# Kernel tuning notes

Hardware: AMD Instinct MI355X
Metric: run time of the kernel (lower is better)

Reference implementation:

```python
import jax, jax.numpy as jnp
import numpy as np
import math

D_MODEL = 1024
N_HEADS = 16
D_HEAD = D_MODEL // N_HEADS
LSR_RANK = 32
B, T = 4, 2048


def setup_inputs() -> dict:
    key = jax.random.key(0)
    ks = jax.random.split(key, 11)
    s = 1.0 / math.sqrt(D_MODEL)
    x = jax.random.normal(ks[0], (B, T, D_MODEL), dtype=jnp.float32)
    Wq = jax.random.uniform(ks[1], (D_MODEL, D_MODEL), minval=-s, maxval=s)
    bq = jax.random.uniform(ks[2], (D_MODEL,), minval=-s, maxval=s)
    Wk = jax.random.uniform(ks[3], (D_MODEL, D_MODEL), minval=-s, maxval=s)
    bk = jax.random.uniform(ks[4], (D_MODEL,), minval=-s, maxval=s)
    Wv = jax.random.uniform(ks[5], (D_MODEL, D_MODEL), minval=-s, maxval=s)
    bv = jax.random.uniform(ks[6], (D_MODEL,), minval=-s, maxval=s)
    Wo = jax.random.uniform(ks[7], (D_MODEL, D_MODEL), minval=-s, maxval=s)
    bo = jax.random.uniform(ks[8], (D_MODEL,), minval=-s, maxval=s)
    Wq_lsr = jax.random.normal(ks[9], (N_HEADS, D_HEAD, LSR_RANK)) / math.sqrt(D_HEAD)
    Wk_lsr = jax.random.normal(ks[10], (N_HEADS, D_HEAD, LSR_RANK)) / math.sqrt(D_HEAD)
    return {"x": x, "Wq": Wq, "bq": bq, "Wk": Wk, "bk": bk,
            "Wv": Wv, "bv": bv, "Wo": Wo, "bo": bo,
            "Wq_lsr": Wq_lsr, "Wk_lsr": Wk_lsr}


def reference(x, Wq, bq, Wk, bk, Wv, bv, Wo, bo, Wq_lsr, Wk_lsr):
    Bq, Tq, _ = x.shape
    # Linear projections (torch Linear: x @ W.T + b), split into heads -> (B,H,T,Dh)
    def split_heads(y):
        return y.reshape(Bq, Tq, N_HEADS, D_HEAD).transpose(0, 2, 1, 3)
    q = split_heads(x @ Wq.T + bq)
    k = split_heads(x @ Wk.T + bk)
    v = split_heads(x @ Wv.T + bv)
    # LSR: project q,k to rank-R per head
    q_lr = jnp.einsum('bhtd,hdr->bhtr', q, Wq_lsr)
    k_lr = jnp.einsum('bhtd,hdr->bhtr', k, Wk_lsr)
    scale = 1.0 / math.sqrt(max(LSR_RANK, 1))
    scores = jnp.einsum('bhir,bhjr->bhij', q_lr, k_lr) * scale  # (B,H,T,T)
    causal_mask = jnp.triu(jnp.ones((Tq, Tq), dtype=bool), k=1)
    scores = jnp.where(causal_mask, jnp.float32(-jnp.inf), scores)
    attn = jax.nn.softmax(scores, axis=-1)
    y = jnp.einsum('bhij,bhjd->bhid', attn, v)  # (B,H,T,Dh)
    y = y.transpose(0, 2, 1, 3).reshape(Bq, Tq, D_MODEL)
    return y @ Wo.T + bo
```

## Files before the change

kernel.cpp:

```cpp
#include <hip/hip_runtime.h>

#define B_  4
#define T_  2048
#define H_  16
#define DM_ 1024
#define DH_ 64
#define RK_ 32

using u16 = unsigned short;
using u32 = unsigned int;
typedef float  floatx4 __attribute__((ext_vector_type(4)));
typedef __bf16 bf16x8  __attribute__((ext_vector_type(8)));
typedef u16    u16x8   __attribute__((ext_vector_type(8)));
typedef u16    u16x4   __attribute__((ext_vector_type(4)));
typedef short  s16x4   __attribute__((ext_vector_type(4)));

#define MFMA16(a,b,c) __builtin_amdgcn_mfma_f32_16x16x32_bf16((a),(b),(c),0,0,0)
#define MFMA1K(a,b,c) __builtin_amdgcn_mfma_f32_16x16x16bf16_1k((a),(b),(c),0,0,0)

__device__ __forceinline__ u16 f2bf(float f) {
  unsigned u = __float_as_uint(f);
  u += 0x7fffu + ((u >> 16) & 1u);
  return (u16)(u >> 16);
}
__device__ __forceinline__ u32 pack_bf(float a, float b) {
  u32 ua = __float_as_uint(a); ua += 0x7fffu + ((ua >> 16) & 1u);
  u32 ub = __float_as_uint(b); ub += 0x7fffu + ((ub >> 16) & 1u);
  return __builtin_amdgcn_perm(ub, ua, 0x07060302u);
}
__device__ __forceinline__ u32 tpack(float a, float b) {
  return __builtin_amdgcn_perm(__float_as_uint(b), __float_as_uint(a), 0x07060302u);
}

__device__ __forceinline__ void async_copy16(const u16* g, const u16* lds_uniform_base) {
  __builtin_amdgcn_global_load_lds(
      (const __attribute__((address_space(1))) unsigned int*)(unsigned long long)g,
      (__attribute__((address_space(3))) unsigned int*)(unsigned int)(unsigned long long)lds_uniform_base,
      16, 0, 0);
}

__global__ __launch_bounds__(256) void cvt_x(const float* __restrict__ s,
                                             u16* __restrict__ d, int n4) {
  int i = blockIdx.x * 256 + threadIdx.x;
  if (i >= n4) return;
  float4 v = reinterpret_cast<const float4*>(s)[i];
  u16x4 o = { f2bf(v.x), f2bf(v.y), f2bf(v.z), f2bf(v.w) };
  reinterpret_cast<u16x4*>(d)[i] = o;
}

__global__ __launch_bounds__(256) void cvt_wvo(const float* __restrict__ Wv,
                                               const float* __restrict__ Wo,
                                               u16* __restrict__ Wcat) {
  int i = blockIdx.x * 256 + threadIdx.x;
  int reg = i >> 18;
  const float* s = reg ? Wo : Wv;
  int j = i & 262143;
  float4 v = reinterpret_cast<const float4*>(s)[j];
  u16x4 o = { f2bf(v.x), f2bf(v.y), f2bf(v.z), f2bf(v.w) };
  reinterpret_cast<u16x4*>(Wcat)[(reg ? 524288 : 0) + j] = o;
}

__global__ __launch_bounds__(256) void lsr_fold(const float* __restrict__ W,
                                                const float* __restrict__ bias,
                                                const float* __restrict__ lsr,
                                                float fold,
                                                u16* __restrict__ Weff,
                                                float* __restrict__ beff) {
  const int hr = blockIdx.x;
  const int h = hr >> 5, r = hr & 31;
  const int tid = threadIdx.x;
  __shared__ float lw[64];
  if (tid < 64) lw[tid] = lsr[(size_t)(h * 64 + tid) * 32 + r] * fold;
  __syncthreads();
  float a0 = 0.f, a1 = 0.f, a2 = 0.f, a3 = 0.f;
  for (int d = 0; d < 64; d++) {
    float l = lw[d];
    float4 wv = *reinterpret_cast<const float4*>(W + (size_t)(h * 64 + d) * 1024 + tid * 4);
    a0 += l * wv.x; a1 += l * wv.y; a2 += l * wv.z; a3 += l * wv.w;
  }
  u16x4 o = { f2bf(a0), f2bf(a1), f2bf(a2), f2bf(a3) };
  reinterpret_cast<u16x4*>(Weff)[(size_t)hr * 256 + tid] = o;
  if (tid == 0) {
    float s = 0.f;
    for (int d = 0; d < 64; d++) s += lw[d] * bias[h * 64 + d];
    beff[hr] = s;
  }
}

template <int MODE>
__global__ __launch_bounds__(256, 2) void gemm8(const u16* __restrict__ A,
                                                const u16* __restrict__ W,
                                                const float* __restrict__ b0,
                                                const float* __restrict__ b1,
                                                const float* __restrict__ b2,
                                                void* __restrict__ Cv,
                                                u16* __restrict__ qo,
                                                u16* __restrict__ ko,
                                                int ldc) {
  __shared__ __align__(16) u16 Al[2][8192];
  __shared__ __align__(16) u16 Bl[2][8192];
  const int tid  = threadIdx.x;
  const int lane = tid & 63;
  const int w    = tid >> 6;
  const int quad = lane >> 4;
  const int l16  = lane & 15;
  const int wm   = (w >> 1) << 6;
  const int wn   = (w & 1) << 6;

  const int bm = blockIdx.x << 7;
  const int bn = blockIdx.y << 7;

  const int sr = tid >> 3;
  const int sc = ((tid & 7) ^ (sr & 7)) * 8;
  const u16* Ag = A + (size_t)(bm + sr) * 1024 + sc;
  const u16* Wg = W + (size_t)(bn + sr) * 1024 + sc;

  auto stage = [&](int k0, int bsel) {
#pragma unroll
    for (int j = 0; j < 4; j++)
      async_copy16(Ag + (size_t)j * 32768 + k0, &Al[bsel][j * 2048 + w * 512]);
#pragma unroll
    for (int j = 0; j < 4; j++)
      async_copy16(Wg + (size_t)j * 32768 + k0, &Bl[bsel][j * 2048 + w * 512]);
  };

  int aoff[4], boff[4], sl[2];
#pragma unroll
  for (int mi = 0; mi < 4; mi++) aoff[mi] = (wm + mi * 16 + l16) * 64;
#pragma unroll
  for (int ni = 0; ni < 4; ni++) boff[ni] = (wn + ni * 16 + l16) * 64;
  sl[0] = ((0 + quad) ^ (l16 & 7)) * 8;
  sl[1] = ((4 + quad) ^ (l16 & 7)) * 8;

  floatx4 acc[4][4];
#pragma unroll
  for (int i = 0; i < 4; i++)
#pragma unroll
    for (int j = 0; j < 4; j++) acc[i][j] = (floatx4){0.f, 0.f, 0.f, 0.f};

  stage(0, 0);
  asm volatile("s_waitcnt vmcnt(0)" ::: "memory");
  __builtin_amdgcn_s_barrier();
  asm volatile("" ::: "memory");

  for (int i = 0; i < 16; i++) {
    if (i < 15) stage((i + 1) * 64, (i + 1) & 1);
    const u16* Ab = Al[i & 1];
    const u16* Bb = Bl[i & 1];
#pragma unroll
    for (int ks = 0; ks < 2; ks++) {
      bf16x8 af[4], bfr[4];
#pragma unroll
      for (int mi = 0; mi < 4; mi++)
        af[mi] = *reinterpret_cast<const bf16x8*>(Ab + aoff[mi] + sl[ks]);
#pragma unroll
      for (int ni = 0; ni < 4; ni++)
        bfr[ni] = *reinterpret_cast<const bf16x8*>(Bb + boff[ni] + sl[ks]);
      __builtin_amdgcn_s_setprio(1);
#pragma unroll
      for (int mi = 0; mi < 4; mi++)
#pragma unroll
        for (int ni = 0; ni < 4; ni++)
          acc[mi][ni] = MFMA16(af[mi], bfr[ni], acc[mi][ni]);
      __builtin_amdgcn_s_setprio(0);
    }
    if (i < 15) {
      asm volatile("s_waitcnt vmcnt(0)" ::: "memory");
      __builtin_amdgcn_s_barrier();
      asm volatile("" ::: "memory");
    }
  }

  if (MODE == 1) {
#pragma unroll
    for (int ni = 0; ni < 4; ni++) {
      int col = bn + wn + ni * 16 + l16;
      float bias = b0[col & 1023];
#pragma unroll
      for (int mi = 0; mi < 4; mi++)
#pragma unroll
        for (int r = 0; r < 4; r++) {
          int row = bm + wm + mi * 16 + quad * 4 + r;
          reinterpret_cast<float*>(Cv)[(size_t)row * ldc + col] = acc[mi][ni][r] + bias;
        }
    }
  } else {
    if (bn < 1024) {
#pragma unroll
      for (int ni = 0; ni < 4; ni++) {
        int col = bn + wn + ni * 16 + l16;
        float bias = b0[col];
#pragma unroll
        for (int mi = 0; mi < 4; mi++)
#pragma unroll
          for (int r = 0; r < 4; r++) {
            int row = bm + wm + mi * 16 + quad * 4 + r;
            reinterpret_cast<u16*>(Cv)[(size_t)row * 1024 + col] =
                f2bf(acc[mi][ni][r] + bias);
          }
      }
    } else {
      u16* outp = (bn < 1536) ? qo : ko;
      const float* bp = (bn < 1536) ? b1 : b2;
#pragma unroll
      for (int ni = 0; ni < 4; ni++) {
        int cc = (bn + wn + ni * 16 + l16) & 511;
        float bias = bp[cc];
        int hh = cc >> 5, rk = cc & 31;
#pragma unroll
        for (int mi = 0; mi < 4; mi++)
#pragma unroll
          for (int r = 0; r < 4; r++) {
            int row = bm + wm + mi * 16 + quad * 4 + r;
            size_t addr =
                ((size_t)((row >> 11) * 16 + hh) * 2048 + (row & 2047)) * 32 + rk;
            outp[addr] = f2bf(acc[mi][ni][r] + bias);
          }
      }
    }
  }
}

__global__ __launch_bounds__(256) void vtrans(const u16* __restrict__ V,
                                              u16* __restrict__ vt) {
  const int tb = blockIdx.x;
  const int bh = blockIdx.y;
  const int b = bh >> 4, h = bh & 15;
  __shared__ u16 Vl[64][72];
  const int tid = threadIdx.x;
#pragma unroll
  for (int it = 0; it < 2; it++) {
    int c = it * 256 + tid;
    int t = c >> 3, dc = (c & 7) * 8;
    u16x8 v = *reinterpret_cast<const u16x8*>(
        V + (size_t)(b * T_ + tb * 64 + t) * 1024 + h * 64 + dc);
    *reinterpret_cast<u16x8*>(&Vl[t][dc]) = v;
  }
  __syncthreads();
#pragma unroll
  for (int it = 0; it < 2; it++) {
    int c = it * 256 + tid;
    int d = c >> 3, tt = (c & 7) * 8;
    u16x8 o;
#pragma unroll
    for (int j = 0; j < 8; j++) o[j] = Vl[tt + j][d];
    *reinterpret_cast<u16x8*>(vt + ((size_t)bh * 64 + d) * T_ + tb * 64 + tt) = o;
  }
}

__global__ __launch_bounds__(256, 4) void attn(const u16* __restrict__ qlr,
                                               const u16* __restrict__ klr,
                                               const u16* __restrict__ vt,
                                               u16* __restrict__ yatt) {
  const int bh = blockIdx.x;
  const int b = bh >> 4, h = bh & 15;
  const int p = blockIdx.y;
  const int tid = threadIdx.x, lane = tid & 63, w = tid >> 6;
  const int quad = lane >> 4, l16 = lane & 15;

  __shared__ __align__(16) u16 Vt3[3][4096];
  __shared__ __align__(16) u16 Kt3[3][2048];

  const u16* qlr_bh = qlr + (size_t)bh * T_ * RK_;
  const u16* klr_bh = klr + (size_t)bh * T_ * RK_;
  const u16* vt_bh  = vt + (size_t)bh * 64 * T_;

  int voff[4][4];
#pragma unroll
  for (int nt = 0; nt < 4; nt++)
#pragma unroll
    for (int dt = 0; dt < 4; dt++) {
      int d = dt * 16 + l16;
      voff[nt][dt] = d * 64 + (((nt * 2 + (quad >> 1)) ^ (d & 7)) * 8) + (quad & 1) * 4;
    }
  int soffV[2];
#pragma unroll
  for (int issue = 0; issue < 2; issue++) {
    int L = issue * 256 + tid;
    int d = L >> 3, cg = L & 7;
    soffV[issue] = d * T_ + ((cg ^ (d & 7)) * 8);
  }
  const int soffK = (w * 8 + (lane >> 3)) * 64 + (((lane & 7) ^ (lane >> 3)) * 8);
  const int koff = (l16 >> 1) * 64 + ((((l16 & 1) * 4 + quad) ^ (l16 >> 1)) * 8);
  const int wub = w * 512;

  const floatx4 fzero = {0.f, 0.f, 0.f, 0.f};

  for (int run = 0; run < 2; run++) {
    const int qi = run ? p : 31 - p;
    const int q0 = qi * 64;
    if (run) __syncthreads();

    bf16x8 qf = *reinterpret_cast<const bf16x8*>(
        qlr_bh + (size_t)(q0 + w * 16 + l16) * 32 + quad * 8);

    auto stage = [&](int t, int bi) {
      const u16* vs = vt_bh + t * 64;
      async_copy16(vs + soffV[0], &Vt3[bi][wub]);
      async_copy16(vs + soffV[1], &Vt3[bi][2048 + wub]);
      async_copy16(klr_bh + t * 2048 + soffK, &Kt3[bi][wub]);
    };

    stage(0, 0);
    if (qi >= 1) {
      stage(1, 1);
      asm volatile("s_waitcnt vmcnt(3)" ::: "memory");
    } else {
      asm volatile("s_waitcnt vmcnt(0)" ::: "memory");
    }
    __builtin_amdgcn_s_barrier();
    asm volatile("" ::: "memory");

    floatx4 oacc[4];
#pragma unroll
    for (int i = 0; i < 4; i++) oacc[i] = fzero;
    float rs = 0.f;

    const u16* Vb = &Vt3[0][0];
    const u16* Kb = &Kt3[0][0];
    int cb = 0, sb = 2;

    for (int i = 0; i < qi; i++) {
      const bool do_stage = (i + 2 <= qi);
      if (do_stage) stage(i + 2, sb);

      bf16x8 kf[4];
#pragma unroll
      for (int nt = 0; nt < 4; nt++)
        kf[nt] = *reinterpret_cast<const bf16x8*>(Kb + koff + nt * 512);
      floatx4 sv[4];
      __builtin_amdgcn_s_setprio(1);
#pragma unroll
      for (int nt = 0; nt < 4; nt++) sv[nt] = MFMA16(kf[nt], qf, fzero);
      __builtin_amdgcn_s_setprio(0);

      uint2 pk[4];
#pragma unroll
      for (int nt = 0; nt < 4; nt++) {
        float p0 = __builtin_amdgcn_exp2f(sv[nt][0]);
        float p1 = __builtin_amdgcn_exp2f(sv[nt][1]);
        float p2 = __builtin_amdgcn_exp2f(sv[nt][2]);
        float p3 = __builtin_amdgcn_exp2f(sv[nt][3]);
        rs += (p0 + p1) + (p2 + p3);
        pk[nt].x = tpack(p0, p1);
        pk[nt].y = tpack(p2, p3);
      }
      __builtin_amdgcn_s_setprio(1);
#pragma unroll
      for (int dt = 0; dt < 4; dt++)
#pragma unroll
        for (int nt = 0; nt < 4; nt++) {
          s16x4 vf = *reinterpret_cast<const s16x4*>(Vb + voff[nt][dt]);
          oacc[dt] = MFMA1K(vf, __builtin_bit_cast(s16x4, pk[nt]), oacc[dt]);
        }
      __builtin_amdgcn_s_setprio(0);

      if (do_stage) asm volatile("s_waitcnt vmcnt(3)" ::: "memory");
      else          asm volatile("s_waitcnt vmcnt(0)" ::: "memory");
      __builtin_amdgcn_s_barrier();
      asm volatile("" ::: "memory");

      cb = (cb == 2) ? 0 : cb + 1;
      Vb = &Vt3[cb][0];
      Kb = &Kt3[cb][0];
      if (do_stage) sb = (sb == 2) ? 0 : sb + 1;
    }

    {
      bf16x8 kf[4];
#pragma unroll
      for (int nt = 0; nt < 4; nt++)
        kf[nt] = *reinterpret_cast<const bf16x8*>(Kb + koff + nt * 512);
      floatx4 sv[4];
#pragma unroll
      for (int nt = 0; nt < 4; nt++) sv[nt] = MFMA16(kf[nt], qf, fzero);
      const int thr = w * 16 + l16;
      uint2 pk[4];
#pragma unroll
      for (int nt = 0; nt < 4; nt++) {
        float pr[4];
#pragma unroll
        for (int r = 0; r < 4; r++) {
          float e = __builtin_amdgcn_exp2f(sv[nt][r]);
          pr[r] = (nt * 16 + quad * 4 + r <= thr) ? e : 0.f;
        }
        rs += (pr[0] + pr[1]) + (pr[2] + pr[3]);
        pk[nt].x = tpack(pr[0], pr[1]);
        pk[nt].y = tpack(pr[2], pr[3]);
      }
      __builtin_amdgcn_s_setprio(1);
#pragma unroll
      for (int dt = 0; dt < 4; dt++)
#pragma unroll
        for (int nt = 0; nt < 4; nt++) {
          s16x4 vf = *reinterpret_cast<const s16x4*>(Vb + voff[nt][dt]);
          oacc[dt] = MFMA1K(vf, __builtin_bit_cast(s16x4, pk[nt]), oacc[dt]);
        }
      __builtin_amdgcn_s_setprio(0);
    }

    rs += __shfl_xor(rs, 16);
    rs += __shfl_xor(rs, 32);
    float inv = 1.f / rs;
    const int qrow = q0 + w * 16 + l16;
#pragma unroll
    for (int dt = 0; dt < 4; dt++) {
      uint2 ov = { pack_bf(oacc[dt][0] * inv, oacc[dt][1] * inv),
                   pack_bf(oacc[dt][2] * inv, oacc[dt][3] * inv) };
      *reinterpret_cast<uint2*>(
          yatt + (size_t)(b * T_ + qrow) * 1024 + h * 64 + dt * 16 + quad * 4) = ov;
    }
  }
}

extern "C" void kernel_launch(void* const* d_in, const int* in_sizes, int n_in,
                              void* d_out, int out_size, void* d_ws, size_t ws_size,
                              hipStream_t stream) {
  const float* x   = (const float*)d_in[0];
  const float* Wq  = (const float*)d_in[1];
  const float* bq  = (const float*)d_in[2];
  const float* Wk  = (const float*)d_in[3];
  const float* bk  = (const float*)d_in[4];
  const float* Wv  = (const float*)d_in[5];
  const float* bv  = (const float*)d_in[6];
  const float* Wo  = (const float*)d_in[7];
  const float* bo  = (const float*)d_in[8];
  const float* Wql = (const float*)d_in[9];
  const float* Wkl = (const float*)d_in[10];
  float* out = (float*)d_out;

  char* ws = (char*)d_ws;
  u16*   xb    = (u16*)(ws);
  u16*   Wcat  = (u16*)(ws + 16777216);
  float* beffq = (float*)(ws + 23068672);
  float* beffk = (float*)(ws + 23072768);
  u16*   Vbuf  = (u16*)(ws + 25165824);
  u16*   qlr   = (u16*)(ws + 41943040);
  u16*   klr   = (u16*)(ws + 50331648);
  u16*   yatt  = (u16*)(ws + 58720256);
  u16*   vt    = xb;

  const float foldq = 0.25506100790944405f;

  cvt_x<<<dim3(8192), 256, 0, stream>>>(x, xb, 2097152);
  cvt_wvo<<<dim3(2048), 256, 0, stream>>>(Wv, Wo, Wcat);
  lsr_fold<<<dim3(512), 256, 0, stream>>>(Wq, bq, Wql, foldq, Wcat + 1048576, beffq);
  lsr_fold<<<dim3(512), 256, 0, stream>>>(Wk, bk, Wkl, 1.0f, Wcat + 1572864, beffk);
  gemm8<2><<<dim3(64, 16), 256, 0, stream>>>(xb, Wcat, bv, beffq, beffk,
                                             Vbuf, qlr, klr, 0);
  vtrans<<<dim3(32, 64), 256, 0, stream>>>(Vbuf, vt);
  attn<<<dim3(64, 16), 256, 0, stream>>>(qlr, klr, vt, yatt);
  gemm8<1><<<dim3(64, 8), 256, 0, stream>>>(yatt, Wcat + 2097152, bo, bo, bo,
                                            out, nullptr, nullptr, 1024);
}
```

Before: 235.3 us.

## Split attention work across waves by key subtile and reduce outputs through LDS

Each wave now owns a 16-key slice of every 64-key tile and computes scores for all four 16-query groups, instead of owning 16 queries across all keys. This cuts per-wave K/V LDS fragment reads (one K fragment and four V fragments per tile instead of four and sixteen) at the cost of four times the accumulator registers (sixteen output accumulators). A cross-wave reduction of partial outputs and row sums through reused LDS buffers, with extra barriers, is added at the end of each run. Register pressure under launch_bounds(256,4) may cause spills or reduce occupancy.

```diff
diff --git a/kernel.cpp b/kernel.cpp
--- a/kernel.cpp
+++ b/kernel.cpp
@@ -265,14 +265,12 @@
   const u16* klr_bh = klr + (size_t)bh * T_ * RK_;
   const u16* vt_bh  = vt + (size_t)bh * 64 * T_;
 
-  int voff[4][4];
-#pragma unroll
-  for (int nt = 0; nt < 4; nt++)
-#pragma unroll
-    for (int dt = 0; dt < 4; dt++) {
-      int d = dt * 16 + l16;
-      voff[nt][dt] = d * 64 + (((nt * 2 + (quad >> 1)) ^ (d & 7)) * 8) + (quad & 1) * 4;
-    }
+  int voffw[4];
+#pragma unroll
+  for (int dt = 0; dt < 4; dt++) {
+    int d = dt * 16 + l16;
+    voffw[dt] = d * 64 + (((w * 2 + (quad >> 1)) ^ (d & 7)) * 8) + (quad & 1) * 4;
+  }
   int soffV[2];
 #pragma unroll
   for (int issue = 0; issue < 2; issue++) {
@@ -281,18 +279,23 @@
     soffV[issue] = d * T_ + ((cg ^ (d & 7)) * 8);
   }
   const int soffK = (w * 8 + (lane >> 3)) * 64 + (((lane & 7) ^ (lane >> 3)) * 8);
-  const int koff = (l16 >> 1) * 64 + ((((l16 & 1) * 4 + quad) ^ (l16 >> 1)) * 8);
+  const int koffw = (l16 >> 1) * 64 + ((((l16 & 1) * 4 + quad) ^ (l16 >> 1)) * 8) + w * 512;
   const int wub = w * 512;
 
   const floatx4 fzero = {0.f, 0.f, 0.f, 0.f};
+  float* oxf = (float*)&Vt3[0][0];
+  float* rsx = (float*)&Kt3[0][0];
 
   for (int run = 0; run < 2; run++) {
     const int qi = run ? p : 31 - p;
     const int q0 = qi * 64;
     if (run) __syncthreads();
 
-    bf16x8 qf = *reinterpret_cast<const bf16x8*>(
-        qlr_bh + (size_t)(q0 + w * 16 + l16) * 32 + quad * 8);
+    bf16x8 qf[4];
+#pragma unroll
+    for (int qg = 0; qg < 4; qg++)
+      qf[qg] = *reinterpret_cast<const bf16x8*>(
+          qlr_bh + (size_t)(q0 + qg * 16 + l16) * 32 + quad * 8);
 
     auto stage = [&](int t, int bi) {
       const u16* vs = vt_bh + t * 64;
@@ -311,10 +314,12 @@
     __builtin_amdgcn_s_barrier();
     asm volatile("" ::: "memory");
 
-    floatx4 oacc[4];
-#pragma unroll
-    for (int i = 0; i < 4; i++) oacc[i] = fzero;
-    float rs = 0.f;
+    floatx4 oacc[4][4];
+#pragma unroll
+    for (int i = 0; i < 4; i++)
+#pragma unroll
+      for (int j = 0; j < 4; j++) oacc[i][j] = fzero;
+    float rs[4] = {0.f, 0.f, 0.f, 0.f};
 
     const u16* Vb = &Vt3[0][0];
     const u16* Kb = &Kt3[0][0];
@@ -324,35 +329,29 @@
       const bool do_stage = (i + 2 <= qi);
       if (do_stage) stage(i + 2, sb);
 
-      bf16x8 kf[4];
-#pragma unroll
-      for (int nt = 0; nt < 4; nt++)
-        kf[nt] = *reinterpret_cast<const bf16x8*>(Kb + koff + nt * 512);
-      floatx4 sv[4];
+      bf16x8 kf = *reinterpret_cast<const bf16x8*>(Kb + koffw);
+      uint2 pk[4];
+#pragma unroll
+      for (int qg = 0; qg < 4; qg++) {
+        __builtin_amdgcn_s_setprio(1);
+        floatx4 sv = MFMA16(kf, qf[qg], fzero);
+        __builtin_amdgcn_s_setprio(0);
+        float p0 = __builtin_amdgcn_exp2f(sv[0]);
+        float p1 = __builtin_amdgcn_exp2f(sv[1]);
+        float p2 = __builtin_amdgcn_exp2f(sv[2]);
+        float p3 = __builtin_amdgcn_exp2f(sv[3]);
+        rs[qg] += (p0 + p1) + (p2 + p3);
+        pk[qg].x = tpack(p0, p1);
+        pk[qg].y = tpack(p2, p3);
+      }
       __builtin_amdgcn_s_setprio(1);
 #pragma unroll
-      for (int nt = 0; nt < 4; nt++) sv[nt] = MFMA16(kf[nt], qf, fzero);
-      __builtin_amdgcn_s_setprio(0);
-
-      uint2 pk[4];
-#pragma unroll
-      for (int nt = 0; nt < 4; nt++) {
-        float p0 = __builtin_amdgcn_exp2f(sv[nt][0]);
-        float p1 = __builtin_amdgcn_exp2f(sv[nt][1]);
-        float p2 = __builtin_amdgcn_exp2f(sv[nt][2]);
-        float p3 = __builtin_amdgcn_exp2f(sv[nt][3]);
-        rs += (p0 + p1) + (p2 + p3);
-        pk[nt].x = tpack(p0, p1);
-        pk[nt].y = tpack(p2, p3);
-      }
-      __builtin_amdgcn_s_setprio(1);
-#pragma unroll
-      for (int dt = 0; dt < 4; dt++)
-#pragma unroll
-        for (int nt = 0; nt < 4; nt++) {
-          s16x4 vf = *reinterpret_cast<const s16x4*>(Vb + voff[nt][dt]);
-          oacc[dt] = MFMA1K(vf, __builtin_bit_cast(s16x4, pk[nt]), oacc[dt]);
-        }
+      for (int dt = 0; dt < 4; dt++) {
+        s16x4 vf = *reinterpret_cast<const s16x4*>(Vb + voffw[dt]);
+#pragma unroll
+        for (int qg = 0; qg < 4; qg++)
+          oacc[dt][qg] = MFMA1K(vf, __builtin_bit_cast(s16x4, pk[qg]), oacc[dt][qg]);
+      }
       __builtin_amdgcn_s_setprio(0);
 
       if (do_stage) asm volatile("s_waitcnt vmcnt(3)" ::: "memory");
@@ -367,48 +366,111 @@
     }
 
     {
-      bf16x8 kf[4];
-#pragma unroll
-      for (int nt = 0; nt < 4; nt++)
-        kf[nt] = *reinterpret_cast<const bf16x8*>(Kb + koff + nt * 512);
-      floatx4 sv[4];
-#pragma unroll
-      for (int nt = 0; nt < 4; nt++) sv[nt] = MFMA16(kf[nt], qf, fzero);
-      const int thr = w * 16 + l16;
+      bf16x8 kf = *reinterpret_cast<const bf16x8*>(Kb + koffw);
+      const int keyl = w * 16 + quad * 4;
       uint2 pk[4];
 #pragma unroll
-      for (int nt = 0; nt < 4; nt++) {
+      for (int qg = 0; qg < 4; qg++) {
+        floatx4 sv = MFMA16(kf, qf[qg], fzero);
+        const int thr = qg * 16 + l16;
         float pr[4];
 #pragma unroll
         for (int r = 0; r < 4; r++) {
-          float e = __builtin_amdgcn_exp2f(sv[nt][r]);
-          pr[r] = (nt * 16 + quad * 4 + r <= thr) ? e : 0.f;
+          float e = __builtin_amdgcn_exp2f(sv[r]);
+          pr[r] = (keyl + r <= thr) ? e : 0.f;
         }
-        rs += (pr[0] + pr[1]) + (pr[2] + pr[3]);
-        pk[nt].x = tpack(pr[0], pr[1]);
-        pk[nt].y = tpack(pr[2], pr[3]);
+        rs[qg] += (pr[0] + pr[1]) + (pr[2] + pr[3]);
+        pk[qg].x = tpack(pr[0], pr[1]);
+        pk[qg].y = tpack(pr[2], pr[3]);
       }
       __builtin_amdgcn_s_setprio(1);
 #pragma unroll
-      for (int dt = 0; dt < 4; dt++)
-#pragma unroll
-        for (int nt = 0; nt < 4; nt++) {
-          s16x4 vf = *reinterpret_cast<const s16x4*>(Vb + voff[nt][dt]);
-          oacc[dt] = MFMA1K(vf, __builtin_bit_cast(s16x4, pk[nt]), oacc[dt]);
+      for (int dt = 0; dt < 4; dt++) {
+        s16x4 vf = *reinterpret_cast<const s16x4*>(Vb + voffw[dt]);
+#pragma unroll
+        for (int qg = 0; qg < 4; qg++)
+          oacc[dt][qg] = MFMA1K(vf, __builtin_bit_cast(s16x4, pk[qg]), oacc[dt][qg]);
+      }
+      __builtin_amdgcn_s_setprio(0);
+    }
+
+#pragma unroll
+    for (int qg = 0; qg < 4; qg++) {
+      rs[qg] += __shfl_xor(rs[qg], 16);
+      rs[qg] += __shfl_xor(rs[qg], 32);
+    }
+
+    __syncthreads();
+    floatx4 ofin[4];
+    float inv[4];
+#pragma unroll
+    for (int dtl = 0; dtl < 2; dtl++) {
+      if (w != dtl) {
+        int ws = w - (w > dtl ? 1 : 0);
+#pragma unroll
+        for (int qg = 0; qg < 4; qg++)
+          *reinterpret_cast<floatx4*>(&oxf[dtl * 3072 + ws * 1024 + qg * 256 + lane * 4]) =
+              oacc[dtl][qg];
+      }
+    }
+    if (quad == 0) {
+#pragma unroll
+      for (int qg = 0; qg < 4; qg++) rsx[(qg * 16 + l16) * 4 + w] = rs[qg];
+    }
+    __syncthreads();
+#pragma unroll
+    for (int dtl = 0; dtl < 2; dtl++) {
+      if (w == dtl) {
+#pragma unroll
+        for (int qg = 0; qg < 4; qg++) {
+          floatx4 s = oacc[dtl][qg];
+#pragma unroll
+          for (int ws = 0; ws < 3; ws++)
+            s += *reinterpret_cast<const floatx4*>(
+                &oxf[dtl * 3072 + ws * 1024 + qg * 256 + lane * 4]);
+          ofin[qg] = s;
         }
-      __builtin_amdgcn_s_setprio(0);
-    }
-
-    rs += __shfl_xor(rs, 16);
-    rs += __shfl_xor(rs, 32);
-    float inv = 1.f / rs;
-    const int qrow = q0 + w * 16 + l16;
-#pragma unroll
-    for (int dt = 0; dt < 4; dt++) {
-      uint2 ov = { pack_bf(oacc[dt][0] * inv, oacc[dt][1] * inv),
-                   pack_bf(oacc[dt][2] * inv, oacc[dt][3] * inv) };
+      }
+    }
+#pragma unroll
+    for (int qg = 0; qg < 4; qg++) {
+      float4 rv = *reinterpret_cast<const float4*>(&rsx[(qg * 16 + l16) * 4]);
+      inv[qg] = 1.f / ((rv.x + rv.y) + (rv.z + rv.w));
+    }
+    __syncthreads();
+#pragma unroll
+    for (int dtl = 2; dtl < 4; dtl++) {
+      if (w != dtl) {
+        int ws = w - (w > dtl ? 1 : 0);
+#pragma unroll
+        for (int qg = 0; qg < 4; qg++)
+          *reinterpret_cast<floatx4*>(&oxf[(dtl & 1) * 3072 + ws * 1024 + qg * 256 + lane * 4]) =
+              oacc[dtl][qg];
+      }
+    }
+    __syncthreads();
+#pragma unroll
+    for (int dtl = 2; dtl < 4; dtl++) {
+      if (w == dtl) {
+#pragma unroll
+        for (int qg = 0; qg < 4; qg++) {
+          floatx4 s = oacc[dtl][qg];
+#pragma unroll
+          for (int ws = 0; ws < 3; ws++)
+            s += *reinterpret_cast<const floatx4*>(
+                &oxf[(dtl & 1) * 3072 + ws * 1024 + qg * 256 + lane * 4]);
+          ofin[qg] = s;
+        }
+      }
+    }
+
+#pragma unroll
+    for (int qg = 0; qg < 4; qg++) {
+      int q = q0 + qg * 16 + l16;
+      uint2 ov = { pack_bf(ofin[qg][0] * inv[qg], ofin[qg][1] * inv[qg]),
+                   pack_bf(ofin[qg][2] * inv[qg], ofin[qg][3] * inv[qg]) };
       *reinterpret_cast<uint2*>(
-          yatt + (size_t)(b * T_ + qrow) * 1024 + h * 64 + dt * 16 + quad * 4) = ov;
+          yatt + (size_t)(b * T_ + q) * 1024 + h * 64 + w * 16 + quad * 4) = ov;
     }
   }
 }
```

New measurement: 258.6 us. 1.1x slower.

## Process two 64-row query groups per warp to reuse staged K/V tiles

Applied to the files above, without the earlier changes.

The attention kernel now handles a 128-row query tile per block iteration, with each warp computing two 16-row query groups against every staged K/V tile. This halves the number of K/V tile loads and barriers per query row, and the grid shrinks from 16 to 8 pairs of query tiles. The diagonal is split into two tiles with masking for each group, and launch bounds drop to 2 blocks per CU to make room for the doubled accumulators. The risks are lower occupancy and fewer blocks to spread across the GPU.

```diff
diff --git a/kernel.cpp b/kernel.cpp
--- a/kernel.cpp
+++ b/kernel.cpp
@@ -248,7 +248,7 @@
   }
 }
 
-__global__ __launch_bounds__(256, 4) void attn(const u16* __restrict__ qlr,
+__global__ __launch_bounds__(256, 2) void attn(const u16* __restrict__ qlr,
                                                const u16* __restrict__ klr,
                                                const u16* __restrict__ vt,
                                                u16* __restrict__ yatt) {
@@ -285,14 +285,19 @@
   const int wub = w * 512;
 
   const floatx4 fzero = {0.f, 0.f, 0.f, 0.f};
+  const int thrq = w * 16 + l16;
 
   for (int run = 0; run < 2; run++) {
-    const int qi = run ? p : 31 - p;
-    const int q0 = qi * 64;
+    const int j = run ? p : 15 - p;
+    const int q0 = j << 7;
+    const int nfull = 2 * j;
     if (run) __syncthreads();
 
-    bf16x8 qf = *reinterpret_cast<const bf16x8*>(
-        qlr_bh + (size_t)(q0 + w * 16 + l16) * 32 + quad * 8);
+    bf16x8 qf[2];
+#pragma unroll
+    for (int qg = 0; qg < 2; qg++)
+      qf[qg] = *reinterpret_cast<const bf16x8*>(
+          qlr_bh + (size_t)(q0 + qg * 64 + thrq) * 32 + quad * 8);
 
     auto stage = [&](int t, int bi) {
       const u16* vs = vt_bh + t * 64;
@@ -302,48 +307,48 @@
     };
 
     stage(0, 0);
-    if (qi >= 1) {
-      stage(1, 1);
-      asm volatile("s_waitcnt vmcnt(3)" ::: "memory");
-    } else {
-      asm volatile("s_waitcnt vmcnt(0)" ::: "memory");
-    }
+    stage(1, 1);
+    asm volatile("s_waitcnt vmcnt(3)" ::: "memory");
     __builtin_amdgcn_s_barrier();
     asm volatile("" ::: "memory");
 
-    floatx4 oacc[4];
-#pragma unroll
-    for (int i = 0; i < 4; i++) oacc[i] = fzero;
-    float rs = 0.f;
+    floatx4 oacc[4][2];
+#pragma unroll
+    for (int i = 0; i < 4; i++)
+#pragma unroll
+      for (int jg = 0; jg < 2; jg++) oacc[i][jg] = fzero;
+    float rs[2] = {0.f, 0.f};
 
     const u16* Vb = &Vt3[0][0];
     const u16* Kb = &Kt3[0][0];
     int cb = 0, sb = 2;
 
-    for (int i = 0; i < qi; i++) {
-      const bool do_stage = (i + 2 <= qi);
-      if (do_stage) stage(i + 2, sb);
+    for (int i = 0; i < nfull; i++) {
+      stage(i + 2, sb);
 
       bf16x8 kf[4];
 #pragma unroll
       for (int nt = 0; nt < 4; nt++)
         kf[nt] = *reinterpret_cast<const bf16x8*>(Kb + koff + nt * 512);
-      floatx4 sv[4];
-      __builtin_amdgcn_s_setprio(1);
-#pragma unroll
-      for (int nt = 0; nt < 4; nt++) sv[nt] = MFMA16(kf[nt], qf, fzero);
-      __builtin_amdgcn_s_setprio(0);
-
-      uint2 pk[4];
-#pragma unroll
-      for (int nt = 0; nt < 4; nt++) {
-        float p0 = __builtin_amdgcn_exp2f(sv[nt][0]);
-        float p1 = __builtin_amdgcn_exp2f(sv[nt][1]);
-        float p2 = __builtin_amdgcn_exp2f(sv[nt][2]);
-        float p3 = __builtin_amdgcn_exp2f(sv[nt][3]);
-        rs += (p0 + p1) + (p2 + p3);
-        pk[nt].x = tpack(p0, p1);
-        pk[nt].y = tpack(p2, p3);
+
+      uint2 pk[4][2];
+#pragma unroll
+      for (int qg = 0; qg < 2; qg++) {
+        __builtin_amdgcn_s_setprio(1);
+        floatx4 sv[4];
+#pragma unroll
+        for (int nt = 0; nt < 4; nt++) sv[nt] = MFMA16(kf[nt], qf[qg], fzero);
+        __builtin_amdgcn_s_setprio(0);
+#pragma unroll
+        for (int nt = 0; nt < 4; nt++) {
+          float p0 = __builtin_amdgcn_exp2f(sv[nt][0]);
+          float p1 = __builtin_amdgcn_exp2f(sv[nt][1]);
+          float p2 = __builtin_amdgcn_exp2f(sv[nt][2]);
+          float p3 = __builtin_amdgcn_exp2f(sv[nt][3]);
+          rs[qg] += (p0 + p1) + (p2 + p3);
+          pk[nt][qg].x = tpack(p0, p1);
+          pk[nt][qg].y = tpack(p2, p3);
+        }
       }
       __builtin_amdgcn_s_setprio(1);
 #pragma unroll
@@ -351,19 +356,19 @@
 #pragma unroll
         for (int nt = 0; nt < 4; nt++) {
           s16x4 vf = *reinterpret_cast<const s16x4*>(Vb + voff[nt][dt]);
-          oacc[dt] = MFMA1K(vf, __builtin_bit_cast(s16x4, pk[nt]), oacc[dt]);
+          oacc[dt][0] = MFMA1K(vf, __builtin_bit_cast(s16x4, pk[nt][0]), oacc[dt][0]);
+          oacc[dt][1] = MFMA1K(vf, __builtin_bit_cast(s16x4, pk[nt][1]), oacc[dt][1]);
         }
       __builtin_amdgcn_s_setprio(0);
 
-      if (do_stage) asm volatile("s_waitcnt vmcnt(3)" ::: "memory");
-      else          asm volatile("s_waitcnt vmcnt(0)" ::: "memory");
+      asm volatile("s_waitcnt vmcnt(3)" ::: "memory");
       __builtin_amdgcn_s_barrier();
       asm volatile("" ::: "memory");
 
       cb = (cb == 2) ? 0 : cb + 1;
       Vb = &Vt3[cb][0];
       Kb = &Kt3[cb][0];
-      if (do_stage) sb = (sb == 2) ? 0 : sb + 1;
+      sb = (sb == 2) ? 0 : sb + 1;
     }
 
     {
@@ -371,20 +376,71 @@
 #pragma unroll
       for (int nt = 0; nt < 4; nt++)
         kf[nt] = *reinterpret_cast<const bf16x8*>(Kb + koff + nt * 512);
-      floatx4 sv[4];
-#pragma unroll
-      for (int nt = 0; nt < 4; nt++) sv[nt] = MFMA16(kf[nt], qf, fzero);
-      const int thr = w * 16 + l16;
+
+      uint2 pk[4][2];
+#pragma unroll
+      for (int nt = 0; nt < 4; nt++) {
+        floatx4 sv = MFMA16(kf[nt], qf[0], fzero);
+        const int keyl = nt * 16 + quad * 4;
+        float pr[4];
+#pragma unroll
+        for (int r = 0; r < 4; r++) {
+          float e = __builtin_amdgcn_exp2f(sv[r]);
+          pr[r] = (keyl + r <= thrq) ? e : 0.f;
+        }
+        rs[0] += (pr[0] + pr[1]) + (pr[2] + pr[3]);
+        pk[nt][0].x = tpack(pr[0], pr[1]);
+        pk[nt][0].y = tpack(pr[2], pr[3]);
+      }
+#pragma unroll
+      for (int nt = 0; nt < 4; nt++) {
+        floatx4 sv = MFMA16(kf[nt], qf[1], fzero);
+        float p0 = __builtin_amdgcn_exp2f(sv[0]);
+        float p1 = __builtin_amdgcn_exp2f(sv[1]);
+        float p2 = __builtin_amdgcn_exp2f(sv[2]);
+        float p3 = __builtin_amdgcn_exp2f(sv[3]);
+        rs[1] += (p0 + p1) + (p2 + p3);
+        pk[nt][1].x = tpack(p0, p1);
+        pk[nt][1].y = tpack(p2, p3);
+      }
+      __builtin_amdgcn_s_setprio(1);
+#pragma unroll
+      for (int dt = 0; dt < 4; dt++)
+#pragma unroll
+        for (int nt = 0; nt < 4; nt++) {
+          s16x4 vf = *reinterpret_cast<const s16x4*>(Vb + voff[nt][dt]);
+          oacc[dt][0] = MFMA1K(vf, __builtin_bit_cast(s16x4, pk[nt][0]), oacc[dt][0]);
+          oacc[dt][1] = MFMA1K(vf, __builtin_bit_cast(s16x4, pk[nt][1]), oacc[dt][1]);
+        }
+      __builtin_amdgcn_s_setprio(0);
+
+      asm volatile("s_waitcnt vmcnt(0)" ::: "memory");
+      __builtin_amdgcn_s_barrier();
+      asm volatile("" ::: "memory");
+
+      cb = (cb == 2) ? 0 : cb + 1;
+      Vb = &Vt3[cb][0];
+      Kb = &Kt3[cb][0];
+    }
+
+    {
+      bf16x8 kf[4];
+#pragma unroll
+      for (int nt = 0; nt < 4; nt++)
+        kf[nt] = *reinterpret_cast<const bf16x8*>(Kb + koff + nt * 512);
+
       uint2 pk[4];
 #pragma unroll
       for (int nt = 0; nt < 4; nt++) {
+        floatx4 sv = MFMA16(kf[nt], qf[1], fzero);
+        const int keyl = nt * 16 + quad * 4;
         float pr[4];
 #pragma unroll
         for (int r = 0; r < 4; r++) {
-          float e = __builtin_amdgcn_exp2f(sv[nt][r]);
-          pr[r] = (nt * 16 + quad * 4 + r <= thr) ? e : 0.f;
-        }
-        rs += (pr[0] + pr[1]) + (pr[2] + pr[3]);
+          float e = __builtin_amdgcn_exp2f(sv[r]);
+          pr[r] = (keyl + r <= thrq) ? e : 0.f;
+        }
+        rs[1] += (pr[0] + pr[1]) + (pr[2] + pr[3]);
         pk[nt].x = tpack(pr[0], pr[1]);
         pk[nt].y = tpack(pr[2], pr[3]);
       }
@@ -394,21 +450,27 @@
 #pragma unroll
         for (int nt = 0; nt < 4; nt++) {
           s16x4 vf = *reinterpret_cast<const s16x4*>(Vb + voff[nt][dt]);
-          oacc[dt] = MFMA1K(vf, __builtin_bit_cast(s16x4, pk[nt]), oacc[dt]);
+          oacc[dt][1] = MFMA1K(vf, __builtin_bit_cast(s16x4, pk[nt]), oacc[dt][1]);
         }
       __builtin_amdgcn_s_setprio(0);
     }
 
-    rs += __shfl_xor(rs, 16);
-    rs += __shfl_xor(rs, 32);
-    float inv = 1.f / rs;
-    const int qrow = q0 + w * 16 + l16;
-#pragma unroll
-    for (int dt = 0; dt < 4; dt++) {
-      uint2 ov = { pack_bf(oacc[dt][0] * inv, oacc[dt][1] * inv),
-                   pack_bf(oacc[dt][2] * inv, oacc[dt][3] * inv) };
-      *reinterpret_cast<uint2*>(
-          yatt + (size_t)(b * T_ + qrow) * 1024 + h * 64 + dt * 16 + quad * 4) = ov;
+#pragma unroll
+    for (int qg = 0; qg < 2; qg++) {
+      rs[qg] += __shfl_xor(rs[qg], 16);
+      rs[qg] += __shfl_xor(rs[qg], 32);
+    }
+#pragma unroll
+    for (int qg = 0; qg < 2; qg++) {
+      float inv = 1.f / rs[qg];
+      const int qrow = q0 + qg * 64 + thrq;
+#pragma unroll
+      for (int dt = 0; dt < 4; dt++) {
+        uint2 ov = { pack_bf(oacc[dt][qg][0] * inv, oacc[dt][qg][1] * inv),
+                     pack_bf(oacc[dt][qg][2] * inv, oacc[dt][qg][3] * inv) };
+        *reinterpret_cast<uint2*>(
+            yatt + (size_t)(b * T_ + qrow) * 1024 + h * 64 + dt * 16 + quad * 4) = ov;
+      }
     }
   }
 }
@@ -449,7 +511,7 @@
   gemm8<2><<<dim3(64, 16), 256, 0, stream>>>(xb, Wcat, bv, beffq, beffk,
                                              Vbuf, qlr, klr, 0);
   vtrans<<<dim3(32, 64), 256, 0, stream>>>(Vbuf, vt);
-  attn<<<dim3(64, 16), 256, 0, stream>>>(qlr, klr, vt, yatt);
+  attn<<<dim3(64, 8), 256, 0, stream>>>(qlr, klr, vt, yatt);
   gemm8<1><<<dim3(64, 8), 256, 0, stream>>>(yatt, Wcat + 2097152, bo, bo, bo,
                                             out, nullptr, nullptr, 1024);
 }
```

Result: slower. 242.9 us (+3.3%).

## Software-pipeline QK scores one tile ahead of PV in attention; merge weight-prep kernels

Applied to the files above, without the earlier changes.

The attention loop now computes the next tile's QK^T scores and exponentials while issuing the current tile's PV MFMAs, so the exp/pack work overlaps matrix-core work instead of serialising with it. K tiles are prefetched three ahead and V tiles two ahead, with the staging split and wait counts adjusted to match. The cvt_wvo and two lsr_fold launches are merged into one prep_w kernel, saving two launches. In exchange the loop holds more live registers (pk and pkn) and has more complex buffer rotation, which could reduce occupancy.

```diff
diff --git a/kernel.cpp b/kernel.cpp
--- a/kernel.cpp
+++ b/kernel.cpp
@@ -48,28 +48,39 @@
   reinterpret_cast<u16x4*>(d)[i] = o;
 }
 
-__global__ __launch_bounds__(256) void cvt_wvo(const float* __restrict__ Wv,
-                                               const float* __restrict__ Wo,
-                                               u16* __restrict__ Wcat) {
-  int i = blockIdx.x * 256 + threadIdx.x;
-  int reg = i >> 18;
-  const float* s = reg ? Wo : Wv;
-  int j = i & 262143;
-  float4 v = reinterpret_cast<const float4*>(s)[j];
-  u16x4 o = { f2bf(v.x), f2bf(v.y), f2bf(v.z), f2bf(v.w) };
-  reinterpret_cast<u16x4*>(Wcat)[(reg ? 524288 : 0) + j] = o;
-}
-
-__global__ __launch_bounds__(256) void lsr_fold(const float* __restrict__ W,
-                                                const float* __restrict__ bias,
-                                                const float* __restrict__ lsr,
-                                                float fold,
-                                                u16* __restrict__ Weff,
-                                                float* __restrict__ beff) {
-  const int hr = blockIdx.x;
+__global__ __launch_bounds__(256) void prep_w(const float* __restrict__ Wv,
+                                              const float* __restrict__ Wo,
+                                              const float* __restrict__ Wq,
+                                              const float* __restrict__ bq,
+                                              const float* __restrict__ Wql,
+                                              const float* __restrict__ Wk,
+                                              const float* __restrict__ bk,
+                                              const float* __restrict__ Wkl,
+                                              u16* __restrict__ Wcat,
+                                              float* __restrict__ beffq,
+                                              float* __restrict__ beffk) {
+  const int tid = threadIdx.x;
+  const int bid = blockIdx.x;
+  __shared__ float lw[64];
+  if (bid < 2048) {
+    int i = bid * 256 + tid;
+    int reg = i >> 18;
+    const float* s = reg ? Wo : Wv;
+    int j = i & 262143;
+    float4 v = reinterpret_cast<const float4*>(s)[j];
+    u16x4 o = { f2bf(v.x), f2bf(v.y), f2bf(v.z), f2bf(v.w) };
+    reinterpret_cast<u16x4*>(Wcat)[(reg ? 524288 : 0) + j] = o;
+    return;
+  }
+  const int sel = (bid >= 2560);
+  const int hr = bid - (sel ? 2560 : 2048);
   const int h = hr >> 5, r = hr & 31;
-  const int tid = threadIdx.x;
-  __shared__ float lw[64];
+  const float* W    = sel ? Wk : Wq;
+  const float* bias = sel ? bk : bq;
+  const float* lsr  = sel ? Wkl : Wql;
+  const float fold  = sel ? 1.0f : 0.25506100790944405f;
+  u16*   Weff = Wcat + (sel ? 1572864 : 1048576);
+  float* beff = sel ? beffk : beffq;
   if (tid < 64) lw[tid] = lsr[(size_t)(h * 64 + tid) * 32 + r] * fold;
   __syncthreads();
   float a0 = 0.f, a1 = 0.f, a2 = 0.f, a3 = 0.f;
@@ -285,29 +296,33 @@
   const int wub = w * 512;
 
   const floatx4 fzero = {0.f, 0.f, 0.f, 0.f};
+  const int thrq = w * 16 + l16;
+
+  auto stageV = [&](int t, int bi) {
+    const u16* vs = vt_bh + t * 64;
+    async_copy16(vs + soffV[0], &Vt3[bi][wub]);
+    async_copy16(vs + soffV[1], &Vt3[bi][2048 + wub]);
+  };
+  auto stageK = [&](int t, int bi) {
+    async_copy16(klr_bh + t * 2048 + soffK, &Kt3[bi][wub]);
+  };
 
   for (int run = 0; run < 2; run++) {
     const int qi = run ? p : 31 - p;
     const int q0 = qi * 64;
-    if (run) __syncthreads();
+    const int last = qi;
 
     bf16x8 qf = *reinterpret_cast<const bf16x8*>(
-        qlr_bh + (size_t)(q0 + w * 16 + l16) * 32 + quad * 8);
-
-    auto stage = [&](int t, int bi) {
-      const u16* vs = vt_bh + t * 64;
-      async_copy16(vs + soffV[0], &Vt3[bi][wub]);
-      async_copy16(vs + soffV[1], &Vt3[bi][2048 + wub]);
-      async_copy16(klr_bh + t * 2048 + soffK, &Kt3[bi][wub]);
-    };
-
-    stage(0, 0);
-    if (qi >= 1) {
-      stage(1, 1);
-      asm volatile("s_waitcnt vmcnt(3)" ::: "memory");
-    } else {
-      asm volatile("s_waitcnt vmcnt(0)" ::: "memory");
-    }
+        qlr_bh + (size_t)(q0 + thrq) * 32 + quad * 8);
+
+    stageV(0, 0);
+    stageK(0, 0);
+    if (last >= 1) stageK(1, 1);
+    if (last >= 1) stageV(1, 1);
+    if (last >= 2) stageK(2, 2);
+    if (last >= 2)      asm volatile("s_waitcnt vmcnt(3)" ::: "memory");
+    else if (last >= 1) asm volatile("s_waitcnt vmcnt(2)" ::: "memory");
+    else                asm volatile("s_waitcnt vmcnt(0)" ::: "memory");
     __builtin_amdgcn_s_barrier();
     asm volatile("" ::: "memory");
 
@@ -315,94 +330,108 @@
 #pragma unroll
     for (int i = 0; i < 4; i++) oacc[i] = fzero;
     float rs = 0.f;
-
-    const u16* Vb = &Vt3[0][0];
-    const u16* Kb = &Kt3[0][0];
-    int cb = 0, sb = 2;
-
-    for (int i = 0; i < qi; i++) {
-      const bool do_stage = (i + 2 <= qi);
-      if (do_stage) stage(i + 2, sb);
-
-      bf16x8 kf[4];
-#pragma unroll
-      for (int nt = 0; nt < 4; nt++)
-        kf[nt] = *reinterpret_cast<const bf16x8*>(Kb + koff + nt * 512);
-      floatx4 sv[4];
-      __builtin_amdgcn_s_setprio(1);
-#pragma unroll
-      for (int nt = 0; nt < 4; nt++) sv[nt] = MFMA16(kf[nt], qf, fzero);
-      __builtin_amdgcn_s_setprio(0);
-
-      uint2 pk[4];
+    uint2 pk[4], pkn[4];
+
+    {
+      const u16* Kb = &Kt3[0][0];
 #pragma unroll
       for (int nt = 0; nt < 4; nt++) {
-        float p0 = __builtin_amdgcn_exp2f(sv[nt][0]);
-        float p1 = __builtin_amdgcn_exp2f(sv[nt][1]);
-        float p2 = __builtin_amdgcn_exp2f(sv[nt][2]);
-        float p3 = __builtin_amdgcn_exp2f(sv[nt][3]);
-        rs += (p0 + p1) + (p2 + p3);
-        pk[nt].x = tpack(p0, p1);
-        pk[nt].y = tpack(p2, p3);
+        bf16x8 kf = *reinterpret_cast<const bf16x8*>(Kb + koff + nt * 512);
+        floatx4 sv = MFMA16(kf, qf, fzero);
+        if (last == 0) {
+          const int keyl = nt * 16 + quad * 4;
+          float pr[4];
+#pragma unroll
+          for (int r = 0; r < 4; r++) {
+            float e = __builtin_amdgcn_exp2f(sv[r]);
+            pr[r] = (keyl + r <= thrq) ? e : 0.f;
+          }
+          rs += (pr[0] + pr[1]) + (pr[2] + pr[3]);
+          pk[nt].x = tpack(pr[0], pr[1]);
+          pk[nt].y = tpack(pr[2], pr[3]);
+        } else {
+          float p0 = __builtin_amdgcn_exp2f(sv[0]);
+          float p1 = __builtin_amdgcn_exp2f(sv[1]);
+          float p2 = __builtin_amdgcn_exp2f(sv[2]);
+          float p3 = __builtin_amdgcn_exp2f(sv[3]);
+          rs += (p0 + p1) + (p2 + p3);
+          pk[nt].x = tpack(p0, p1);
+          pk[nt].y = tpack(p2, p3);
+        }
       }
-      __builtin_amdgcn_s_setprio(1);
-#pragma unroll
-      for (int dt = 0; dt < 4; dt++)
+    }
+
+    int cb = 0, cb1 = 1, cb2 = 2;
+
+    for (int i = 0; i <= last; i++) {
+      const bool sV = (i + 2 <= last);
+      const bool sK = (i + 3 <= last);
+      if (sV) stageV(i + 2, cb2);
+      if (sK) stageK(i + 3, cb);
+      const u16* Vb = &Vt3[cb][0];
+
+      if (i + 1 <= last) {
+        const u16* Kb = &Kt3[cb1][0];
+        const bool maskNext = (i + 1 == last);
 #pragma unroll
         for (int nt = 0; nt < 4; nt++) {
-          s16x4 vf = *reinterpret_cast<const s16x4*>(Vb + voff[nt][dt]);
-          oacc[dt] = MFMA1K(vf, __builtin_bit_cast(s16x4, pk[nt]), oacc[dt]);
+          bf16x8 kf = *reinterpret_cast<const bf16x8*>(Kb + koff + nt * 512);
+          __builtin_amdgcn_s_setprio(1);
+          floatx4 sv = MFMA16(kf, qf, fzero);
+#pragma unroll
+          for (int dt = 0; dt < 4; dt++) {
+            s16x4 vf = *reinterpret_cast<const s16x4*>(Vb + voff[nt][dt]);
+            oacc[dt] = MFMA1K(vf, __builtin_bit_cast(s16x4, pk[nt]), oacc[dt]);
+          }
+          __builtin_amdgcn_s_setprio(0);
+          if (maskNext) {
+            const int keyl = nt * 16 + quad * 4;
+            float pr[4];
+#pragma unroll
+            for (int r = 0; r < 4; r++) {
+              float e = __builtin_amdgcn_exp2f(sv[r]);
+              pr[r] = (keyl + r <= thrq) ? e : 0.f;
+            }
+            rs += (pr[0] + pr[1]) + (pr[2] + pr[3]);
+            pkn[nt].x = tpack(pr[0], pr[1]);
+            pkn[nt].y = tpack(pr[2], pr[3]);
+          } else {
+            float p0 = __builtin_amdgcn_exp2f(sv[0]);
+            float p1 = __builtin_amdgcn_exp2f(sv[1]);
+            float p2 = __builtin_amdgcn_exp2f(sv[2]);
+            float p3 = __builtin_amdgcn_exp2f(sv[3]);
+            rs += (p0 + p1) + (p2 + p3);
+            pkn[nt].x = tpack(p0, p1);
+            pkn[nt].y = tpack(p2, p3);
+          }
         }
-      __builtin_amdgcn_s_setprio(0);
-
-      if (do_stage) asm volatile("s_waitcnt vmcnt(3)" ::: "memory");
-      else          asm volatile("s_waitcnt vmcnt(0)" ::: "memory");
+#pragma unroll
+        for (int nt = 0; nt < 4; nt++) pk[nt] = pkn[nt];
+      } else {
+        __builtin_amdgcn_s_setprio(1);
+#pragma unroll
+        for (int nt = 0; nt < 4; nt++)
+#pragma unroll
+          for (int dt = 0; dt < 4; dt++) {
+            s16x4 vf = *reinterpret_cast<const s16x4*>(Vb + voff[nt][dt]);
+            oacc[dt] = MFMA1K(vf, __builtin_bit_cast(s16x4, pk[nt]), oacc[dt]);
+          }
+        __builtin_amdgcn_s_setprio(0);
+      }
+
+      if (sK)      asm volatile("s_waitcnt vmcnt(3)" ::: "memory");
+      else if (sV) asm volatile("s_waitcnt vmcnt(2)" ::: "memory");
+      else         asm volatile("s_waitcnt vmcnt(0)" ::: "memory");
       __builtin_amdgcn_s_barrier();
       asm volatile("" ::: "memory");
 
-      cb = (cb == 2) ? 0 : cb + 1;
-      Vb = &Vt3[cb][0];
-      Kb = &Kt3[cb][0];
-      if (do_stage) sb = (sb == 2) ? 0 : sb + 1;
-    }
-
-    {
-      bf16x8 kf[4];
-#pragma unroll
-      for (int nt = 0; nt < 4; nt++)
-        kf[nt] = *reinterpret_cast<const bf16x8*>(Kb + koff + nt * 512);
-      floatx4 sv[4];
-#pragma unroll
-      for (int nt = 0; nt < 4; nt++) sv[nt] = MFMA16(kf[nt], qf, fzero);
-      const int thr = w * 16 + l16;
-      uint2 pk[4];
-#pragma unroll
-      for (int nt = 0; nt < 4; nt++) {
-        float pr[4];
-#pragma unroll
-        for (int r = 0; r < 4; r++) {
-          float e = __builtin_amdgcn_exp2f(sv[nt][r]);
-          pr[r] = (nt * 16 + quad * 4 + r <= thr) ? e : 0.f;
-        }
-        rs += (pr[0] + pr[1]) + (pr[2] + pr[3]);
-        pk[nt].x = tpack(pr[0], pr[1]);
-        pk[nt].y = tpack(pr[2], pr[3]);
-      }
-      __builtin_amdgcn_s_setprio(1);
-#pragma unroll
-      for (int dt = 0; dt < 4; dt++)
-#pragma unroll
-        for (int nt = 0; nt < 4; nt++) {
-          s16x4 vf = *reinterpret_cast<const s16x4*>(Vb + voff[nt][dt]);
-          oacc[dt] = MFMA1K(vf, __builtin_bit_cast(s16x4, pk[nt]), oacc[dt]);
-        }
-      __builtin_amdgcn_s_setprio(0);
+      int t = cb; cb = cb1; cb1 = cb2; cb2 = t;
     }
 
     rs += __shfl_xor(rs, 16);
     rs += __shfl_xor(rs, 32);
     float inv = 1.f / rs;
-    const int qrow = q0 + w * 16 + l16;
+    const int qrow = q0 + thrq;
 #pragma unroll
     for (int dt = 0; dt < 4; dt++) {
       uint2 ov = { pack_bf(oacc[dt][0] * inv, oacc[dt][1] * inv),
@@ -440,12 +469,9 @@
   u16*   yatt  = (u16*)(ws + 58720256);
   u16*   vt    = xb;
 
-  const float foldq = 0.25506100790944405f;
-
   cvt_x<<<dim3(8192), 256, 0, stream>>>(x, xb, 2097152);
-  cvt_wvo<<<dim3(2048), 256, 0, stream>>>(Wv, Wo, Wcat);
-  lsr_fold<<<dim3(512), 256, 0, stream>>>(Wq, bq, Wql, foldq, Wcat + 1048576, beffq);
-  lsr_fold<<<dim3(512), 256, 0, stream>>>(Wk, bk, Wkl, 1.0f, Wcat + 1572864, beffk);
+  prep_w<<<dim3(3072), 256, 0, stream>>>(Wv, Wo, Wq, bq, Wql, Wk, bk, Wkl,
+                                         Wcat, beffq, beffk);
   gemm8<2><<<dim3(64, 16), 256, 0, stream>>>(xb, Wcat, bv, beffq, beffk,
                                              Vbuf, qlr, klr, 0);
   vtrans<<<dim3(32, 64), 256, 0, stream>>>(Vbuf, vt);
```

Result: slower. 249.6 us (+6.1%).
